# Kernel optimization log

Measured on AMD Instinct MI355X. Metric: run time of the kernel, lower is better.

The kernel has to match this reference:

```python
import jax, jax.numpy as jnp
import numpy as np

T_IN, B, H = 24, 8192, 512
T_OUT, OVERLAP, PE_DIM = 12, 4, 4

def setup_inputs() -> dict:
    key = jax.random.key(0)
    ks = jax.random.split(key, 10)
    s = 1.0 / np.sqrt(H)
    return {
        "encoder_out": jax.random.normal(ks[0], (T_IN, B, H), jnp.float32),
        "encoder_hid": jax.random.normal(ks[1], (B, H), jnp.float32),
        "last": jax.random.normal(ks[2], (B, OVERLAP), jnp.float32),
        "pos_embed": jax.random.normal(ks[3], (T_OUT, PE_DIM), jnp.float32),
        "W_ih": jax.random.uniform(ks[4], (3 * H, OVERLAP + PE_DIM), jnp.float32, -s, s),
        "W_hh": jax.random.uniform(ks[5], (3 * H, H), jnp.float32, -s, s),
        "b_ih": jax.random.uniform(ks[6], (3 * H,), jnp.float32, -s, s),
        "b_hh": jax.random.uniform(ks[7], (3 * H,), jnp.float32, -s, s),
        "W_lin": jax.random.uniform(ks[8], (1, 2 * H), jnp.float32, -s, s),
        "b_lin": jax.random.uniform(ks[9], (1,), jnp.float32, -s, s),
    }

def reference(encoder_out, encoder_hid, last, pos_embed, W_ih, W_hh, b_ih, b_hh, W_lin, b_lin):
    batch = encoder_hid.shape[0]
    n_out = pos_embed.shape[0]
    overlap = last.shape[1]

    def gru_cell(x, h):
        gi = x @ W_ih.T + b_ih          # (B, 3H)
        gh = h @ W_hh.T + b_hh          # (B, 3H)
        i_r, i_z, i_n = jnp.split(gi, 3, axis=-1)
        h_r, h_z, h_n = jnp.split(gh, 3, axis=-1)
        r = jax.nn.sigmoid(i_r + h_r)
        z = jax.nn.sigmoid(i_z + h_z)
        n = jnp.tanh(i_n + r * h_n)
        return (1.0 - z) * n + z * h

    def step_fn(carry, step):
        hidden, last_in = carry
        # Bahdanau-style additive attention over encoder timesteps
        attn = jnp.einsum('tbh,bh->tb', encoder_out, hidden)
        attn = jax.nn.softmax(attn, axis=0)
        context = jnp.einsum('tbh,tb->bh', encoder_out, attn)  # (B, H)
        hidden = hidden + context
        pe = jnp.broadcast_to(pos_embed[step], (batch, pos_embed.shape[1]))
        decode_last = jnp.concatenate([last_in, pe], axis=-1)  # (B, overlap+4)
        hidden = gru_cell(decode_last, hidden)
        out = jnp.concatenate([hidden, context], axis=-1) @ W_lin.T + b_lin  # (B, 1)
        new_last = jnp.concatenate(
            [jax.lax.stop_gradient(out), last_in[:, : overlap - 1]], axis=-1)
        return (hidden, new_last), out[:, 0]

    (_, _), outs = jax.lax.scan(step_fn, (encoder_hid, last), jnp.arange(n_out))
    return outs.T  # (B, num_timesteps_output)
```

## Files before the change

### kernel.cpp

```cpp
#include <hip/hip_runtime.h>

#define T_IN   24
#define NB     8192
#define HD     512
#define T_OUT  12

typedef float  f32x4  __attribute__((ext_vector_type(4)));
typedef short  bf16x8 __attribute__((ext_vector_type(8)));

#define GLD16(g, l) __builtin_amdgcn_global_load_lds( \
    (__attribute__((address_space(1))) void*)(g), \
    (__attribute__((address_space(3))) void*)(l), 16, 0, 0)

__device__ __forceinline__ unsigned short f2bf(float f){
  unsigned u = __float_as_uint(f);
  u += 0x7fffu + ((u >> 16) & 1u);
  return (unsigned short)(u >> 16);
}
__device__ __forceinline__ float bf2f(unsigned short h){
  return __uint_as_float(((unsigned)h) << 16);
}
__device__ __forceinline__ float wsum(float v){
  #pragma unroll
  for (int o = 32; o; o >>= 1) v += __shfl_xor(v, o);
  return v;
}

__global__ __launch_bounds__(256) void conv_whh(const float* __restrict__ W,
                                                unsigned short* __restrict__ hi,
                                                unsigned short* __restrict__ lo){
  int i = blockIdx.x * 256 + threadIdx.x;
  float v = W[i];
  unsigned short h = f2bf(v);
  hi[i] = h;
  lo[i] = f2bf(v - bf2f(h));
}

__global__ __launch_bounds__(256, 4) void attn_step(
    const float* __restrict__ enc,
    const float* __restrict__ hid_in,
    const float* __restrict__ Wlin,
    const float* __restrict__ blin,
    const float* __restrict__ last_init,
    float* __restrict__ last_ws,
    float* __restrict__ ctxdot,
    unsigned short* __restrict__ h2hi,
    unsigned short* __restrict__ h2lo,
    float* __restrict__ outp,
    int step, int rev)
{
  __shared__ float lpart[4][28];
  __shared__ float po_s[4];
  __shared__ float red2[4];
  __shared__ float wts_s[T_IN];

  const int b   = rev ? (NB - 1 - (int)blockIdx.x) : (int)blockIdx.x;
  const int tid = threadIdx.x;
  const int l   = tid & 63;
  const int w   = tid >> 6;
  const int c0  = 2 * tid;

  float2 e[T_IN];
  #pragma unroll
  for (int t = 0; t < T_IN; t++)
    e[t] = *(const float2*)(enc + ((size_t)t * NB + b) * HD + c0);
  float2 hh  = *(const float2*)(hid_in + (size_t)b * HD + c0);
  float2 wl0 = *(const float2*)(Wlin + c0);
  float2 wl1 = *(const float2*)(Wlin + HD + c0);

  float p[T_IN];
  #pragma unroll
  for (int t = 0; t < T_IN; t++) p[t] = e[t].x * hh.x + e[t].y * hh.y;

  float po = hh.x * wl0.x + hh.y * wl0.y;
  po = wsum(po);
  if (l == 0) po_s[w] = po;

  const int b0 = l & 1, b1 = (l >> 1) & 1, b2 = (l >> 2) & 1;
  float q[12];
  #pragma unroll
  for (int j = 0; j < 12; j++){
    float send = b0 ? p[j] : p[12 + j];
    float keep = b0 ? p[12 + j] : p[j];
    q[j] = keep + __shfl_xor(send, 1);
  }
  float r6[6];
  #pragma unroll
  for (int j = 0; j < 6; j++){
    float send = b1 ? q[j] : q[6 + j];
    float keep = b1 ? q[6 + j] : q[j];
    r6[j] = keep + __shfl_xor(send, 2);
  }
  float s3[3];
  #pragma unroll
  for (int j = 0; j < 3; j++){
    float send = b2 ? r6[j] : r6[3 + j];
    float keep = b2 ? r6[3 + j] : r6[j];
    s3[j] = keep + __shfl_xor(send, 4);
  }
  #pragma unroll
  for (int j = 0; j < 3; j++){
    s3[j] += __shfl_xor(s3[j], 8);
    s3[j] += __shfl_xor(s3[j], 16);
    s3[j] += __shfl_xor(s3[j], 32);
  }
  if (l < 8){
    int tb = 12 * b0 + 6 * b1 + 3 * b2;
    lpart[w][tb + 0] = s3[0];
    lpart[w][tb + 1] = s3[1];
    lpart[w][tb + 2] = s3[2];
  }
  __syncthreads();

  if (w == 0){
    float v = -3.0e38f;
    if (l < T_IN) v = lpart[0][l] + lpart[1][l] + lpart[2][l] + lpart[3][l];
    float m = v;
    #pragma unroll
    for (int o = 32; o; o >>= 1) m = fmaxf(m, __shfl_xor(m, o));
    float ex = (l < T_IN) ? exp2f((v - m) * 1.44269504f) : 0.f;
    float s = wsum(ex);
    if (l < T_IN) wts_s[l] = ex / s;
  }
  if (w == 1 && l == 0){
    if (step > 0){
      float val = po_s[0] + po_s[1] + po_s[2] + po_s[3] + ctxdot[b];
      outp[(size_t)b * T_OUT + (step - 1)] = val;
      float4 old = *(const float4*)(last_ws + (size_t)b * 4);
      float4 nl; nl.x = val; nl.y = old.x; nl.z = old.y; nl.w = old.z;
      *(float4*)(last_ws + (size_t)b * 4) = nl;
    } else {
      *(float4*)(last_ws + (size_t)b * 4) = *(const float4*)(last_init + (size_t)b * 4);
    }
  }
  __syncthreads();

  float c0v = 0.f, c1v = 0.f;
  #pragma unroll
  for (int t = 0; t < T_IN; t++){
    float wt = wts_s[t];
    c0v += wt * e[t].x;
    c1v += wt * e[t].y;
  }
  float h20 = hh.x + c0v;
  float h21 = hh.y + c1v;
  size_t base = (size_t)b * HD + c0;
  unsigned short q0 = f2bf(h20), q1 = f2bf(h21);
  *(unsigned int*)(h2hi + base) = (unsigned)q0 | ((unsigned)q1 << 16);
  unsigned short r0 = f2bf(h20 - bf2f(q0)), r1 = f2bf(h21 - bf2f(q1));
  *(unsigned int*)(h2lo + base) = (unsigned)r0 | ((unsigned)r1 << 16);

  float pc = c0v * wl1.x + c1v * wl1.y;
  pc = wsum(pc);
  if (l == 0) red2[w] = pc;
  __syncthreads();
  if (tid == 0) ctxdot[b] = red2[0] + red2[1] + red2[2] + red2[3] + blin[0];
}

__global__ __launch_bounds__(512, 4) void gru_gemm(
    const unsigned short* __restrict__ Ahi,
    const unsigned short* __restrict__ Alo,
    const unsigned short* __restrict__ Bhi,
    const unsigned short* __restrict__ Blo,
    const float* __restrict__ last_ws,
    const float* __restrict__ pe,
    const float* __restrict__ W_ih,
    const float* __restrict__ b_ih,
    const float* __restrict__ b_hh,
    float* __restrict__ hidden,
    int step)
{
  __shared__ __align__(16) unsigned short smem[2 * 20480];
  const int tid = threadIdx.x;
  const int bid = blockIdx.x;
  const int xk  = bid & 7;
  const int sl  = bid >> 3;
  const int xt  = (xk << 3) | (sl >> 3);
  const int yt  = sl & 7;
  const int b0  = xt * 128;
  const int n0  = yt * 64;
  const int l   = tid & 63;
  const int wv  = tid >> 6;
  const int wm  = wv >> 2;
  const int wn  = wv & 3;
  const int lr  = l & 15;
  const int lkb = (l >> 4) << 4;

  f32x4 acc[3][4];
  #pragma unroll
  for (int g = 0; g < 3; g++)
    #pragma unroll
    for (int mi = 0; mi < 4; mi++)
      acc[g][mi] = (f32x4){0.f, 0.f, 0.f, 0.f};

  auto stage = [&](int kt, int buf){
    unsigned short* sb = smem + buf * 20480;
    {
      int row = tid >> 2;
      int pb  = (tid & 3) << 4;
      int ke  = (pb ^ ((row & 3) << 4)) >> 1;
      size_t ga = (size_t)(b0 + row) * HD + kt * 32 + ke;
      GLD16(Ahi + ga, sb + tid * 8);
      GLD16(Alo + ga, sb + 4096 + tid * 8);
    }
    {
      int c = tid;
      int row = c >> 2;
      int pb  = (c & 3) << 4;
      int ke  = (pb ^ ((row & 3) << 4)) >> 1;
      size_t ga = (size_t)((row >> 6) * 512 + n0 + (row & 63)) * HD + kt * 32 + ke;
      GLD16(Bhi + ga, sb + 8192 + c * 8);
      GLD16(Blo + ga, sb + 14336 + c * 8);
      if (tid < 256){
        c = tid + 512;
        row = c >> 2;
        pb  = (c & 3) << 4;
        ke  = (pb ^ ((row & 3) << 4)) >> 1;
        ga  = (size_t)((row >> 6) * 512 + n0 + (row & 63)) * HD + kt * 32 + ke;
        GLD16(Bhi + ga, sb + 8192 + c * 8);
        GLD16(Blo + ga, sb + 14336 + c * 8);
      }
    }
  };

  stage(0, 0);
  for (int kt = 0; kt < 16; kt++){
    const int cur = kt & 1;
    __syncthreads();
    if (kt + 1 < 16) stage(kt + 1, cur ^ 1);
    const unsigned short* sb = smem + cur * 20480;
    bf16x8 ah[4], al[4];
    #pragma unroll
    for (int mi = 0; mi < 4; mi++){
      int row = wm * 64 + mi * 16 + lr;
      int o = row * 32 + ((lkb ^ ((row & 3) << 4)) >> 1);
      ah[mi] = *(const bf16x8*)(sb + o);
      al[mi] = *(const bf16x8*)(sb + 4096 + o);
    }
    #pragma unroll
    for (int g = 0; g < 3; g++){
      int row = g * 64 + wn * 16 + lr;
      int o = row * 32 + ((lkb ^ ((row & 3) << 4)) >> 1);
      bf16x8 bh = *(const bf16x8*)(sb + 8192 + o);
      bf16x8 bl = *(const bf16x8*)(sb + 14336 + o);
      #pragma unroll
      for (int mi = 0; mi < 4; mi++){
        acc[g][mi] = __builtin_amdgcn_mfma_f32_16x16x32_bf16(ah[mi], bh, acc[g][mi], 0, 0, 0);
        acc[g][mi] = __builtin_amdgcn_mfma_f32_16x16x32_bf16(al[mi], bh, acc[g][mi], 0, 0, 0);
        acc[g][mi] = __builtin_amdgcn_mfma_f32_16x16x32_bf16(ah[mi], bl, acc[g][mi], 0, 0, 0);
      }
    }
  }

  const float pe0 = pe[step * 4 + 0], pe1 = pe[step * 4 + 1],
              pe2 = pe[step * 4 + 2], pe3 = pe[step * 4 + 3];
  const int jg = n0 + wn * 16 + lr;
  const float* wrp = W_ih + (size_t)jg * 8;
  const float* wzp = W_ih + (size_t)(512 + jg) * 8;
  const float* wnp = W_ih + (size_t)(1024 + jg) * 8;
  float4 wr0 = *(const float4*)wrp, wr1 = *(const float4*)(wrp + 4);
  float4 wz0 = *(const float4*)wzp, wz1 = *(const float4*)(wzp + 4);
  float4 wn0 = *(const float4*)wnp, wn1 = *(const float4*)(wnp + 4);
  float cr = pe0*wr1.x + pe1*wr1.y + pe2*wr1.z + pe3*wr1.w + b_ih[jg]       + b_hh[jg];
  float cz = pe0*wz1.x + pe1*wz1.y + pe2*wz1.z + pe3*wz1.w + b_ih[512+jg]   + b_hh[512+jg];
  float cn = pe0*wn1.x + pe1*wn1.y + pe2*wn1.z + pe3*wn1.w + b_ih[1024+jg];
  const float bhn = b_hh[1024 + jg];

  #pragma unroll
  for (int mi = 0; mi < 4; mi++){
    #pragma unroll
    for (int q = 0; q < 4; q++){
      int brow = wm * 64 + mi * 16 + ((l >> 4) << 2) + q;
      size_t bg = (size_t)(b0 + brow);
      float4 x = *(const float4*)(last_ws + bg * 4);
      float gr = x.x*wr0.x + x.y*wr0.y + x.z*wr0.z + x.w*wr0.w + cr + acc[0][mi][q];
      float gz = x.x*wz0.x + x.y*wz0.y + x.z*wz0.z + x.w*wz0.w + cz + acc[1][mi][q];
      float gn = x.x*wn0.x + x.y*wn0.y + x.z*wn0.z + x.w*wn0.w + cn;
      float r = 1.f / (1.f + exp2f(-1.44269504f * gr));
      float z = 1.f / (1.f + exp2f(-1.44269504f * gz));
      float nn = gn + r * (acc[2][mi][q] + bhn);
      float th = 1.f - 2.f / (1.f + exp2f(2.88539008f * nn));
      size_t hoff = bg * HD + jg;
      float h = bf2f(Ahi[hoff]) + bf2f(Alo[hoff]);
      hidden[hoff] = (1.f - z) * th + z * h;
    }
  }
}

__global__ __launch_bounds__(256) void final_out(
    const float* __restrict__ hidden, const float* __restrict__ Wlin,
    const float* __restrict__ ctxdot, float* __restrict__ outp)
{
  int tid = threadIdx.x; int l = tid & 63; int w = tid >> 6;
  int b = blockIdx.x * 4 + w;
  const float* hb = hidden + (size_t)b * HD;
  float p = 0.f;
  #pragma unroll
  for (int j = 0; j < 8; j++) p += hb[l + 64 * j] * Wlin[l + 64 * j];
  p = wsum(p);
  if (l == 0) outp[(size_t)b * T_OUT + 11] = p + ctxdot[b];
}

extern "C" void kernel_launch(void* const* d_in, const int* in_sizes, int n_in,
                              void* d_out, int out_size, void* d_ws, size_t ws_size,
                              hipStream_t stream){
  (void)in_sizes; (void)n_in; (void)out_size; (void)ws_size;
  const float* enc   = (const float*)d_in[0];
  const float* ehid  = (const float*)d_in[1];
  const float* last0 = (const float*)d_in[2];
  const float* pe    = (const float*)d_in[3];
  const float* W_ih  = (const float*)d_in[4];
  const float* W_hh  = (const float*)d_in[5];
  const float* b_ih  = (const float*)d_in[6];
  const float* b_hh  = (const float*)d_in[7];
  const float* W_lin = (const float*)d_in[8];
  const float* b_lin = (const float*)d_in[9];
  float* outp = (float*)d_out;

  char* ws = (char*)d_ws;
  size_t off = 0;
  auto alloc = [&](size_t bytes){ void* p = ws + off; off += (bytes + 255) & ~(size_t)255; return p; };
  unsigned short* whh_hi = (unsigned short*)alloc((size_t)1536 * 512 * 2);
  unsigned short* whh_lo = (unsigned short*)alloc((size_t)1536 * 512 * 2);
  unsigned short* h2hi   = (unsigned short*)alloc((size_t)NB * HD * 2);
  unsigned short* h2lo   = (unsigned short*)alloc((size_t)NB * HD * 2);
  float*          hidden = (float*)         alloc((size_t)NB * HD * 4);
  float*          lastw  = (float*)         alloc((size_t)NB * 4 * 4);
  float*          ctxd   = (float*)         alloc((size_t)NB * 4);

  conv_whh<<<3072, 256, 0, stream>>>(W_hh, whh_hi, whh_lo);
  for (int s = 0; s < T_OUT; s++){
    attn_step<<<NB, 256, 0, stream>>>(enc, s == 0 ? ehid : hidden, W_lin, b_lin,
                                      last0, lastw, ctxd, h2hi, h2lo, outp, s, s & 1);
    gru_gemm<<<512, 512, 0, stream>>>(h2hi, h2lo, whh_hi, whh_lo,
                                      lastw, pe, W_ih, b_ih, b_hh, hidden, s);
  }
  final_out<<<2048, 256, 0, stream>>>(hidden, W_lin, ctxd, outp);
}
```

Baseline: 1.436 ms.

## Process batch in two chunks so encoder slice stays cache-resident across steps

The whole 12-step decode now runs separately on two halves of the batch, with workspaces sized for one chunk. The GRU GEMM tile shrinks from 128 to 64 batch rows so the existing 512-block grid still covers a chunk. The aim is to keep each chunk's encoder slice, about 200MB, resident in the large last-level cache across all steps, instead of re-streaming 400MB from HBM every step. The cost is twice as many kernel launches and a smaller GEMM tile with less operand reuse.

```diff
diff --git a/kernel.cpp b/kernel.cpp
--- a/kernel.cpp
+++ b/kernel.cpp
@@ -4,6 +4,7 @@
 #define NB     8192
 #define HD     512
 #define T_OUT  12
+#define CH     4096
 
 typedef float  f32x4  __attribute__((ext_vector_type(4)));
 typedef short  bf16x8 __attribute__((ext_vector_type(8)));
@@ -54,7 +55,7 @@
   __shared__ float red2[4];
   __shared__ float wts_s[T_IN];
 
-  const int b   = rev ? (NB - 1 - (int)blockIdx.x) : (int)blockIdx.x;
+  const int b   = rev ? (CH - 1 - (int)blockIdx.x) : (int)blockIdx.x;
   const int tid = threadIdx.x;
   const int l   = tid & 63;
   const int w   = tid >> 6;
@@ -170,14 +171,14 @@
     float* __restrict__ hidden,
     int step)
 {
-  __shared__ __align__(16) unsigned short smem[2 * 20480];
+  __shared__ __align__(16) unsigned short smem[2 * 16384];
   const int tid = threadIdx.x;
   const int bid = blockIdx.x;
   const int xk  = bid & 7;
   const int sl  = bid >> 3;
   const int xt  = (xk << 3) | (sl >> 3);
   const int yt  = sl & 7;
-  const int b0  = xt * 128;
+  const int b0  = xt * 64;
   const int n0  = yt * 64;
   const int l   = tid & 63;
   const int wv  = tid >> 6;
@@ -186,22 +187,22 @@
   const int lr  = l & 15;
   const int lkb = (l >> 4) << 4;
 
-  f32x4 acc[3][4];
+  f32x4 acc[3][2];
   #pragma unroll
   for (int g = 0; g < 3; g++)
     #pragma unroll
-    for (int mi = 0; mi < 4; mi++)
+    for (int mi = 0; mi < 2; mi++)
       acc[g][mi] = (f32x4){0.f, 0.f, 0.f, 0.f};
 
   auto stage = [&](int kt, int buf){
-    unsigned short* sb = smem + buf * 20480;
-    {
+    unsigned short* sb = smem + buf * 16384;
+    if (tid < 256){
       int row = tid >> 2;
       int pb  = (tid & 3) << 4;
       int ke  = (pb ^ ((row & 3) << 4)) >> 1;
       size_t ga = (size_t)(b0 + row) * HD + kt * 32 + ke;
       GLD16(Ahi + ga, sb + tid * 8);
-      GLD16(Alo + ga, sb + 4096 + tid * 8);
+      GLD16(Alo + ga, sb + 2048 + tid * 8);
     }
     {
       int c = tid;
@@ -209,16 +210,16 @@
       int pb  = (c & 3) << 4;
       int ke  = (pb ^ ((row & 3) << 4)) >> 1;
       size_t ga = (size_t)((row >> 6) * 512 + n0 + (row & 63)) * HD + kt * 32 + ke;
-      GLD16(Bhi + ga, sb + 8192 + c * 8);
-      GLD16(Blo + ga, sb + 14336 + c * 8);
+      GLD16(Bhi + ga, sb + 4096 + c * 8);
+      GLD16(Blo + ga, sb + 10240 + c * 8);
       if (tid < 256){
         c = tid + 512;
         row = c >> 2;
         pb  = (c & 3) << 4;
         ke  = (pb ^ ((row & 3) << 4)) >> 1;
         ga  = (size_t)((row >> 6) * 512 + n0 + (row & 63)) * HD + kt * 32 + ke;
-        GLD16(Bhi + ga, sb + 8192 + c * 8);
-        GLD16(Blo + ga, sb + 14336 + c * 8);
+        GLD16(Bhi + ga, sb + 4096 + c * 8);
+        GLD16(Blo + ga, sb + 10240 + c * 8);
       }
     }
   };
@@ -228,23 +229,23 @@
     const int cur = kt & 1;
     __syncthreads();
     if (kt + 1 < 16) stage(kt + 1, cur ^ 1);
-    const unsigned short* sb = smem + cur * 20480;
-    bf16x8 ah[4], al[4];
-    #pragma unroll
-    for (int mi = 0; mi < 4; mi++){
-      int row = wm * 64 + mi * 16 + lr;
+    const unsigned short* sb = smem + cur * 16384;
+    bf16x8 ah[2], al[2];
+    #pragma unroll
+    for (int mi = 0; mi < 2; mi++){
+      int row = wm * 32 + mi * 16 + lr;
       int o = row * 32 + ((lkb ^ ((row & 3) << 4)) >> 1);
       ah[mi] = *(const bf16x8*)(sb + o);
-      al[mi] = *(const bf16x8*)(sb + 4096 + o);
+      al[mi] = *(const bf16x8*)(sb + 2048 + o);
     }
     #pragma unroll
     for (int g = 0; g < 3; g++){
       int row = g * 64 + wn * 16 + lr;
-      int o = row * 32 + ((lkb ^ ((row & 3) << 4)) >> 1);
-      bf16x8 bh = *(const bf16x8*)(sb + 8192 + o);
-      bf16x8 bl = *(const bf16x8*)(sb + 14336 + o);
+      int o = 4096 + row * 32 + ((lkb ^ ((row & 3) << 4)) >> 1);
+      bf16x8 bh = *(const bf16x8*)(sb + o);
+      bf16x8 bl = *(const bf16x8*)(sb + o + 6144);
       #pragma unroll
-      for (int mi = 0; mi < 4; mi++){
+      for (int mi = 0; mi < 2; mi++){
         acc[g][mi] = __builtin_amdgcn_mfma_f32_16x16x32_bf16(ah[mi], bh, acc[g][mi], 0, 0, 0);
         acc[g][mi] = __builtin_amdgcn_mfma_f32_16x16x32_bf16(al[mi], bh, acc[g][mi], 0, 0, 0);
         acc[g][mi] = __builtin_amdgcn_mfma_f32_16x16x32_bf16(ah[mi], bl, acc[g][mi], 0, 0, 0);
@@ -267,10 +268,10 @@
   const float bhn = b_hh[1024 + jg];
 
   #pragma unroll
-  for (int mi = 0; mi < 4; mi++){
+  for (int mi = 0; mi < 2; mi++){
     #pragma unroll
     for (int q = 0; q < 4; q++){
-      int brow = wm * 64 + mi * 16 + ((l >> 4) << 2) + q;
+      int brow = wm * 32 + mi * 16 + ((l >> 4) << 2) + q;
       size_t bg = (size_t)(b0 + brow);
       float4 x = *(const float4*)(last_ws + bg * 4);
       float gr = x.x*wr0.x + x.y*wr0.y + x.z*wr0.z + x.w*wr0.w + cr + acc[0][mi][q];
@@ -322,18 +323,25 @@
   auto alloc = [&](size_t bytes){ void* p = ws + off; off += (bytes + 255) & ~(size_t)255; return p; };
   unsigned short* whh_hi = (unsigned short*)alloc((size_t)1536 * 512 * 2);
   unsigned short* whh_lo = (unsigned short*)alloc((size_t)1536 * 512 * 2);
-  unsigned short* h2hi   = (unsigned short*)alloc((size_t)NB * HD * 2);
-  unsigned short* h2lo   = (unsigned short*)alloc((size_t)NB * HD * 2);
-  float*          hidden = (float*)         alloc((size_t)NB * HD * 4);
-  float*          lastw  = (float*)         alloc((size_t)NB * 4 * 4);
-  float*          ctxd   = (float*)         alloc((size_t)NB * 4);
+  unsigned short* h2hi   = (unsigned short*)alloc((size_t)CH * HD * 2);
+  unsigned short* h2lo   = (unsigned short*)alloc((size_t)CH * HD * 2);
+  float*          hidden = (float*)         alloc((size_t)CH * HD * 4);
+  float*          lastw  = (float*)         alloc((size_t)CH * 4 * 4);
+  float*          ctxd   = (float*)         alloc((size_t)CH * 4);
 
   conv_whh<<<3072, 256, 0, stream>>>(W_hh, whh_hi, whh_lo);
-  for (int s = 0; s < T_OUT; s++){
-    attn_step<<<NB, 256, 0, stream>>>(enc, s == 0 ? ehid : hidden, W_lin, b_lin,
-                                      last0, lastw, ctxd, h2hi, h2lo, outp, s, s & 1);
-    gru_gemm<<<512, 512, 0, stream>>>(h2hi, h2lo, whh_hi, whh_lo,
-                                      lastw, pe, W_ih, b_ih, b_hh, hidden, s);
-  }
-  final_out<<<2048, 256, 0, stream>>>(hidden, W_lin, ctxd, outp);
-}
+  for (int c = 0; c < NB / CH; c++){
+    const size_t base = (size_t)c * CH;
+    const float* enc_c  = enc   + base * HD;
+    const float* ehid_c = ehid  + base * HD;
+    const float* last_c = last0 + base * 4;
+    float*       outp_c = outp  + base * T_OUT;
+    for (int s = 0; s < T_OUT; s++){
+      attn_step<<<CH, 256, 0, stream>>>(enc_c, s == 0 ? ehid_c : hidden, W_lin, b_lin,
+                                        last_c, lastw, ctxd, h2hi, h2lo, outp_c, s, s & 1);
+      gru_gemm<<<512, 512, 0, stream>>>(h2hi, h2lo, whh_hi, whh_lo,
+                                        lastw, pe, W_ih, b_ih, b_hh, hidden, s);
+    }
+    final_out<<<CH / 4, 256, 0, stream>>>(hidden, W_lin, ctxd, outp_c);
+  }
+}
```

Measured after the change: 1.475 ms. 2.7% more time.

## Load W_hh fragments directly from a k-tiled global layout instead of LDS

Applied to the files above, without the earlier changes.

The W_hh conversion kernel now writes the bf16 hi/lo split in a k-tile-major layout, with 32-element chunks per row grouped by k block. The GRU GEMM stops staging the B operand through LDS and reads each wave's B fragments straight from global memory in that layout. Only A is double-buffered in LDS, which shrinks shared memory per block and could raise occupancy. In exchange, B fragments become uncached-in-LDS global loads that sit on the MFMA critical path without prefetch, relying on L1/L2 hits because several waves share the same rows.

```diff
diff --git a/kernel.cpp b/kernel.cpp
--- a/kernel.cpp
+++ b/kernel.cpp
@@ -29,11 +29,13 @@
 __global__ __launch_bounds__(256) void conv_whh(const float* __restrict__ W,
                                                 unsigned short* __restrict__ hi,
                                                 unsigned short* __restrict__ lo){
-  int i = blockIdx.x * 256 + threadIdx.x;
-  float v = W[i];
+  int idx = blockIdx.x * 256 + threadIdx.x;
+  int j = idx >> 9, k = idx & 511;
+  float v = W[idx];
   unsigned short h = f2bf(v);
-  hi[i] = h;
-  lo[i] = f2bf(v - bf2f(h));
+  int o = ((k >> 5) * 1536 + j) * 32 + (k & 31);
+  hi[o] = h;
+  lo[o] = f2bf(v - bf2f(h));
 }
 
 __global__ __launch_bounds__(256, 4) void attn_step(
@@ -170,7 +172,7 @@
     float* __restrict__ hidden,
     int step)
 {
-  __shared__ __align__(16) unsigned short smem[2 * 20480];
+  __shared__ __align__(16) unsigned short smem[2 * 8192];
   const int tid = threadIdx.x;
   const int bid = blockIdx.x;
   const int xk  = bid & 7;
@@ -193,42 +195,22 @@
     for (int mi = 0; mi < 4; mi++)
       acc[g][mi] = (f32x4){0.f, 0.f, 0.f, 0.f};
 
-  auto stage = [&](int kt, int buf){
-    unsigned short* sb = smem + buf * 20480;
-    {
-      int row = tid >> 2;
-      int pb  = (tid & 3) << 4;
-      int ke  = (pb ^ ((row & 3) << 4)) >> 1;
-      size_t ga = (size_t)(b0 + row) * HD + kt * 32 + ke;
-      GLD16(Ahi + ga, sb + tid * 8);
-      GLD16(Alo + ga, sb + 4096 + tid * 8);
-    }
-    {
-      int c = tid;
-      int row = c >> 2;
-      int pb  = (c & 3) << 4;
-      int ke  = (pb ^ ((row & 3) << 4)) >> 1;
-      size_t ga = (size_t)((row >> 6) * 512 + n0 + (row & 63)) * HD + kt * 32 + ke;
-      GLD16(Bhi + ga, sb + 8192 + c * 8);
-      GLD16(Blo + ga, sb + 14336 + c * 8);
-      if (tid < 256){
-        c = tid + 512;
-        row = c >> 2;
-        pb  = (c & 3) << 4;
-        ke  = (pb ^ ((row & 3) << 4)) >> 1;
-        ga  = (size_t)((row >> 6) * 512 + n0 + (row & 63)) * HD + kt * 32 + ke;
-        GLD16(Bhi + ga, sb + 8192 + c * 8);
-        GLD16(Blo + ga, sb + 14336 + c * 8);
-      }
-    }
+  auto stageA = [&](int kt, int buf){
+    unsigned short* sb = smem + buf * 8192;
+    int row = tid >> 2;
+    int pb  = (tid & 3) << 4;
+    int ke  = (pb ^ ((row & 3) << 4)) >> 1;
+    size_t ga = (size_t)(b0 + row) * HD + kt * 32 + ke;
+    GLD16(Ahi + ga, sb + tid * 8);
+    GLD16(Alo + ga, sb + 4096 + tid * 8);
   };
 
-  stage(0, 0);
+  stageA(0, 0);
   for (int kt = 0; kt < 16; kt++){
     const int cur = kt & 1;
     __syncthreads();
-    if (kt + 1 < 16) stage(kt + 1, cur ^ 1);
-    const unsigned short* sb = smem + cur * 20480;
+    if (kt + 1 < 16) stageA(kt + 1, cur ^ 1);
+    const unsigned short* sb = smem + cur * 8192;
     bf16x8 ah[4], al[4];
     #pragma unroll
     for (int mi = 0; mi < 4; mi++){
@@ -239,10 +221,9 @@
     }
     #pragma unroll
     for (int g = 0; g < 3; g++){
-      int row = g * 64 + wn * 16 + lr;
-      int o = row * 32 + ((lkb ^ ((row & 3) << 4)) >> 1);
-      bf16x8 bh = *(const bf16x8*)(sb + 8192 + o);
-      bf16x8 bl = *(const bf16x8*)(sb + 14336 + o);
+      size_t boff = ((size_t)kt * 1536 + g * 512 + n0 + wn * 16 + lr) * 32 + ((l >> 4) << 3);
+      bf16x8 bh = *(const bf16x8*)(Bhi + boff);
+      bf16x8 bl = *(const bf16x8*)(Blo + boff);
       #pragma unroll
       for (int mi = 0; mi < 4; mi++){
         acc[g][mi] = __builtin_amdgcn_mfma_f32_16x16x32_bf16(ah[mi], bh, acc[g][mi], 0, 0, 0);
```

New measurement: 1.463 ms. Within noise of the previous version (+1.9%).
